# Performance work log

Hardware: AMD Instinct MI355X
Metric: run time of the kernel (lower is better)

## Reference

```python
import jax, jax.numpy as jnp
import numpy as np

NUM_GROUPS = 8   # num_groups1, recursive_index=False path
NUM_HEADS = 8


def setup_inputs() -> dict:
    key = jax.random.key(0)
    k1, k2, k3 = jax.random.split(key, 3)
    B, C, H, W = 4, 256, 64, 64
    x = jax.random.normal(k1, (B, C, H, W), dtype=jnp.float32)
    w_qkv = jax.random.normal(k2, (3 * C, C), dtype=jnp.float32) * 0.02
    w_proj = jax.random.normal(k3, (C, C), dtype=jnp.float32) * 0.02
    b_proj = jnp.zeros((C,), dtype=jnp.float32)
    return {"x": x, "w_qkv": w_qkv, "w_proj": w_proj, "b_proj": b_proj}


def reference(x, w_qkv, w_proj, b_proj):
    B, C, H, W = x.shape
    N = H * W
    G = NUM_GROUPS
    nh = NUM_HEADS
    hd = C // nh
    M = N // G
    scale = hd ** -0.5

    # b c h w -> b (h w) c
    xf = x.reshape(B, C, N).transpose(0, 2, 1)  # [B, N, C]

    # qkv linear (no bias), then split into groups / heads
    qkv = (xf @ w_qkv.T).reshape(B, G, M, 3, nh, hd)
    qkv = jnp.transpose(qkv, (3, 0, 1, 4, 2, 5))  # [3, B, G, nh, M, hd]
    q, k, v = qkv[0], qkv[1], qkv[2]

    # grouped multi-head attention, manual softmax
    attn = jax.nn.softmax(jnp.einsum('bghmd,bghnd->bghmn', q, k) * scale, axis=-1)
    out = jnp.einsum('bghmn,bghnd->bghmd', attn, v)

    # [B,G,nh,M,hd] -> [B,G,M,C] -> [B,N,C]
    out = out.transpose(0, 1, 3, 2, 4).reshape(B, N, C)

    out = out @ w_proj.T + b_proj

    # b (h w) c -> b c h w
    return out.transpose(0, 2, 1).reshape(B, C, H, W)
```

## Files before the change

### kernel.cpp

```cpp
#include <hip/hip_runtime.h>
#include <hip/hip_bf16.h>

#define Bb 4
#define Cc 256
#define Nn 4096
#define Gg 8
#define NHh 8
#define HDd 32
#define Mm 512

typedef __bf16 bf16_t;
typedef __bf16 bf16x2 __attribute__((ext_vector_type(2)));
typedef __bf16 bf16x4 __attribute__((ext_vector_type(4)));
typedef __bf16 bf16x8 __attribute__((ext_vector_type(8)));
typedef float f32x4 __attribute__((ext_vector_type(4)));

#define LSCALE (0.17677669529663687f * 1.44269504088896340f)

__device__ __forceinline__ void load_lds16(const bf16_t* g, bf16_t* l) {
  __builtin_amdgcn_global_load_lds(
      (const __attribute__((address_space(1))) void*)g,
      (__attribute__((address_space(3))) void*)l, 16, 0, 0);
}

__global__ __launch_bounds__(256) void prep_kernel(
    const float* __restrict__ x, bf16_t* __restrict__ xT,
    const float* __restrict__ wqkv, const float* __restrict__ wproj,
    bf16_t* __restrict__ wq_b, bf16_t* __restrict__ wp_b) {
  int bid = blockIdx.x, tid = threadIdx.x;
  if (bid >= 1024) {
    int i = (bid - 1024) * 256 + tid;
    wq_b[i] = (bf16_t)wqkv[i];
    if (i < Cc * Cc) wp_b[i] = (bf16_t)wproj[i];
    return;
  }
  __shared__ float t[64][65];
  int b = bid >> 8, c0 = ((bid >> 6) & 3) * 64, n0 = (bid & 63) * 64;
  const float* xp = x + ((long long)b * Cc + c0) * Nn + n0;
#pragma unroll
  for (int it = 0; it < 4; ++it) {
    int idx = it * 256 + tid;
    int r = idx >> 4, col = (idx & 15) * 4;
    f32x4 v = *(const f32x4*)&xp[(long long)r * Nn + col];
    t[r][col] = v[0];
    t[r][col + 1] = v[1];
    t[r][col + 2] = v[2];
    t[r][col + 3] = v[3];
  }
  __syncthreads();
  bf16_t* op = xT + ((long long)b * Nn + n0) * Cc + c0;
#pragma unroll
  for (int it = 0; it < 2; ++it) {
    int idx = it * 256 + tid;
    int n = idx >> 3, cg = (idx & 7) * 8;
    bf16x8 w;
#pragma unroll
    for (int j = 0; j < 8; ++j) w[j] = (bf16_t)t[cg + j][n];
    *(bf16x8*)&op[(long long)n * Cc + cg] = w;
  }
}

__global__ __launch_bounds__(256) void qkv_gemm_kernel(
    const bf16_t* __restrict__ xT, const bf16_t* __restrict__ wqb,
    bf16_t* __restrict__ Qh, bf16_t* __restrict__ Kh, bf16_t* __restrict__ Vh) {
  __shared__ bf16_t As[128 * 32];
  __shared__ bf16_t Bs[128 * 32];
  int bid = blockIdx.x;
  int tid = threadIdx.x, lane = tid & 63, wid = tid >> 6;
  int quad = lane >> 4, l16 = lane & 15;
  bool isQK = bid < 512;
  const bf16_t *A, *Bt;
  int m0, n0, z = 0;
  if (isQK) {
    m0 = (bid >> 2) * 128;
    n0 = (bid & 3) * 128;
    A = xT;
    Bt = wqb;
  } else {
    int vb = bid - 512;
    z = vb >> 6;
    int rem = vb & 63;
    m0 = (rem >> 5) * 128;
    n0 = (rem & 31) * 128;
    A = wqb + 512 * Cc;
    Bt = xT + (long long)z * Nn * Cc;
  }
  int wm = (wid >> 1) * 64, wn = (wid & 1) * 64;

  f32x4 acc[4][4];
#pragma unroll
  for (int i = 0; i < 4; ++i)
#pragma unroll
    for (int j = 0; j < 4; ++j) acc[i][j] = (f32x4){0.f, 0.f, 0.f, 0.f};

  int scol = (lane & 3) * 8;
  for (int k0 = 0; k0 < Cc; k0 += 32) {
    __syncthreads();
#pragma unroll
    for (int r = 0; r < 2; ++r) {
      int chunk = wid * 2 + r;
      int row = chunk * 16 + (lane >> 2);
      load_lds16(&A[(long long)(m0 + row) * Cc + k0 + scol], &As[chunk * 512]);
      load_lds16(&Bt[(long long)(n0 + row) * Cc + k0 + scol], &Bs[chunk * 512]);
    }
    __syncthreads();
    bf16x8 a[4], b[4];
#pragma unroll
    for (int i = 0; i < 4; ++i)
      a[i] = *(const bf16x8*)&As[(wm + i * 16 + l16) * 32 + quad * 8];
#pragma unroll
    for (int j = 0; j < 4; ++j)
      b[j] = *(const bf16x8*)&Bs[(wn + j * 16 + l16) * 32 + quad * 8];
#pragma unroll
    for (int i = 0; i < 4; ++i)
#pragma unroll
      for (int j = 0; j < 4; ++j)
        acc[i][j] = __builtin_amdgcn_mfma_f32_16x16x32_bf16(a[i], b[j], acc[i][j], 0, 0, 0);
  }

#pragma unroll
  for (int i = 0; i < 4; ++i) {
#pragma unroll
    for (int j = 0; j < 4; ++j) {
      int col = n0 + wn + j * 16 + l16;
#pragma unroll
      for (int r = 0; r < 4; ++r) {
        int row = m0 + wm + i * 16 + quad * 4 + r;
        float v = acc[i][j][r];
        if (isQK) {
          int bb = row >> 12, gg = (row >> 9) & 7, m = row & 511;
          int hh = (col >> 5) & 7, d = col & 31;
          long long hb = (long long)((bb << 6) | (gg << 3) | hh) * (Mm * HDd);
          if (col < 256)
            Qh[hb + m * HDd + d] = (bf16_t)(v * LSCALE);
          else
            Kh[hb + m * HDd + d] = (bf16_t)v;
        } else {
          int hh = row >> 5, d = row & 31, gg = col >> 9, m = col & 511;
          long long hb = (long long)((z << 6) | (gg << 3) | hh) * (Mm * HDd);
          Vh[hb + d * Mm + m] = (bf16_t)v;
        }
      }
    }
  }
}

__global__ __launch_bounds__(256, 2) void attn_kernel(
    const bf16_t* __restrict__ Qh, const bf16_t* __restrict__ Kh,
    const bf16_t* __restrict__ Vh, bf16_t* __restrict__ Oa) {
  __shared__ bf16_t Ks[512 * 32];
  __shared__ bf16_t Vs[32 * 520];
  int gid = blockIdx.x;
  int ms = gid & 1, head = gid >> 1;
  int h = head & 7, g = (head >> 3) & 7, b = head >> 6;
  int tid = threadIdx.x, lane = tid & 63, wid = tid >> 6;
  int quad = lane >> 4, l16 = lane & 15;

  const bf16_t* Kg = Kh + (long long)head * (Mm * HDd);
  const bf16_t* Vg = Vh + (long long)head * (Mm * HDd);
  const bf16_t* Qg = Qh + (long long)head * (Mm * HDd) + ms * 256 * HDd;

#pragma unroll
  for (int it = 0; it < 8; ++it) {
    int chunk = wid * 8 + it;
    load_lds16(&Kg[chunk * 512 + lane * 8], &Ks[chunk * 512]);
  }
#pragma unroll
  for (int it = 0; it < 8; ++it) {
    int d = wid * 8 + it;
    load_lds16(&Vg[d * Mm + lane * 8], &Vs[d * 520]);
  }
  __syncthreads();

  int rp0 = ((l16 >> 2) << 3) | (l16 & 3);
  const bf16_t* Kp0 = &Ks[rp0 * HDd + quad * 8];
  const bf16_t* Kp1 = Kp0 + 4 * HDd;
  const bf16_t* VsL = &Vs[l16 * 520 + quad * 8];
  const bf16_t* VsH = &Vs[(16 + l16) * 520 + quad * 8];
  const f32x4 zero = (f32x4){0.f, 0.f, 0.f, 0.f};

#pragma unroll 1
  for (int t = 0; t < 2; ++t) {
    int m0 = wid * 64 + t * 32;
    bf16x8 qa = *(const bf16x8*)&Qg[(m0 + l16) * HDd + quad * 8];
    bf16x8 qb = *(const bf16x8*)&Qg[(m0 + 16 + l16) * HDd + quad * 8];

    float sma = 0.f, smb = 0.f;
    f32x4 oLa = zero, oHa = zero, oLb = zero, oHb = zero;

#pragma unroll 4
    for (int c = 0; c < 16; ++c) {
      int nb = c * 32;
      bf16x8 kf0 = *(const bf16x8*)&Kp0[nb * HDd];
      bf16x8 kf1 = *(const bf16x8*)&Kp1[nb * HDd];
      f32x4 sa0 = __builtin_amdgcn_mfma_f32_16x16x32_bf16(kf0, qa, zero, 0, 0, 0);
      f32x4 sa1 = __builtin_amdgcn_mfma_f32_16x16x32_bf16(kf1, qa, zero, 0, 0, 0);
      f32x4 sb0 = __builtin_amdgcn_mfma_f32_16x16x32_bf16(kf0, qb, zero, 0, 0, 0);
      f32x4 sb1 = __builtin_amdgcn_mfma_f32_16x16x32_bf16(kf1, qb, zero, 0, 0, 0);
      bf16x8 pa, pb;
#pragma unroll
      for (int r = 0; r < 4; ++r) {
        float e0 = __builtin_exp2f(sa0[r]);
        float e1 = __builtin_exp2f(sa1[r]);
        sma += e0 + e1;
        pa[r] = (bf16_t)e0;
        pa[4 + r] = (bf16_t)e1;
        float f0 = __builtin_exp2f(sb0[r]);
        float f1 = __builtin_exp2f(sb1[r]);
        smb += f0 + f1;
        pb[r] = (bf16_t)f0;
        pb[4 + r] = (bf16_t)f1;
      }
      bf16x8 vL = *(const bf16x8*)&VsL[nb];
      bf16x8 vH = *(const bf16x8*)&VsH[nb];
      oLa = __builtin_amdgcn_mfma_f32_16x16x32_bf16(vL, pa, oLa, 0, 0, 0);
      oHa = __builtin_amdgcn_mfma_f32_16x16x32_bf16(vH, pa, oHa, 0, 0, 0);
      oLb = __builtin_amdgcn_mfma_f32_16x16x32_bf16(vL, pb, oLb, 0, 0, 0);
      oHb = __builtin_amdgcn_mfma_f32_16x16x32_bf16(vH, pb, oHb, 0, 0, 0);
    }

    sma += __shfl_xor(sma, 16, 64);
    sma += __shfl_xor(sma, 32, 64);
    smb += __shfl_xor(smb, 16, 64);
    smb += __shfl_xor(smb, 32, 64);
    float inva = 1.f / sma, invb = 1.f / smb;

    long long orowa =
        ((long long)(b * Nn + g * Mm + ms * 256 + m0 + l16)) * Cc + h * HDd;
    long long orowb = orowa + 16 * Cc;
    bf16x4 wLa, wHa, wLb, wHb;
#pragma unroll
    for (int r = 0; r < 4; ++r) {
      wLa[r] = (bf16_t)(oLa[r] * inva);
      wHa[r] = (bf16_t)(oHa[r] * inva);
      wLb[r] = (bf16_t)(oLb[r] * invb);
      wHb[r] = (bf16_t)(oHb[r] * invb);
    }
    *(bf16x4*)&Oa[orowa + quad * 4] = wLa;
    *(bf16x4*)&Oa[orowa + 16 + quad * 4] = wHa;
    *(bf16x4*)&Oa[orowb + quad * 4] = wLb;
    *(bf16x4*)&Oa[orowb + 16 + quad * 4] = wHb;
  }
}

__global__ __launch_bounds__(256) void proj_kernel(
    const bf16_t* __restrict__ Wp, const bf16_t* __restrict__ Oa,
    float* __restrict__ out, const float* __restrict__ bias) {
  __shared__ bf16_t As[128 * 32];
  __shared__ bf16_t Bs[128 * 32];
  int tid = threadIdx.x, lane = tid & 63, wid = tid >> 6;
  int quad = lane >> 4, l16 = lane & 15;
  int z = blockIdx.z;
  const bf16_t* Bt = Oa + (long long)z * Nn * Cc;
  int m0 = blockIdx.y * 128, n0 = blockIdx.x * 128;
  int wm = (wid >> 1) * 64, wn = (wid & 1) * 64;

  f32x4 acc[4][4];
#pragma unroll
  for (int i = 0; i < 4; ++i)
#pragma unroll
    for (int j = 0; j < 4; ++j) acc[i][j] = (f32x4){0.f, 0.f, 0.f, 0.f};

  int scol = (lane & 3) * 8;
  for (int k0 = 0; k0 < Cc; k0 += 32) {
    __syncthreads();
#pragma unroll
    for (int r = 0; r < 2; ++r) {
      int chunk = wid * 2 + r;
      int row = chunk * 16 + (lane >> 2);
      load_lds16(&Wp[(long long)(m0 + row) * Cc + k0 + scol], &As[chunk * 512]);
      load_lds16(&Bt[(long long)(n0 + row) * Cc + k0 + scol], &Bs[chunk * 512]);
    }
    __syncthreads();
    bf16x8 a[4], b[4];
#pragma unroll
    for (int i = 0; i < 4; ++i)
      a[i] = *(const bf16x8*)&As[(wm + i * 16 + l16) * 32 + quad * 8];
#pragma unroll
    for (int j = 0; j < 4; ++j)
      b[j] = *(const bf16x8*)&Bs[(wn + j * 16 + l16) * 32 + quad * 8];
#pragma unroll
    for (int i = 0; i < 4; ++i)
#pragma unroll
      for (int j = 0; j < 4; ++j)
        acc[i][j] = __builtin_amdgcn_mfma_f32_16x16x32_bf16(a[i], b[j], acc[i][j], 0, 0, 0);
  }

#pragma unroll
  for (int i = 0; i < 4; ++i) {
#pragma unroll
    for (int j = 0; j < 4; ++j) {
      int col = n0 + wn + j * 16 + l16;
#pragma unroll
      for (int r = 0; r < 4; ++r) {
        int row = m0 + wm + i * 16 + quad * 4 + r;
        out[(long long)z * (Cc * Nn) + (long long)row * Nn + col] =
            acc[i][j][r] + bias[row];
      }
    }
  }
}

extern "C" void kernel_launch(void* const* d_in, const int* in_sizes, int n_in,
                              void* d_out, int out_size, void* d_ws, size_t ws_size,
                              hipStream_t stream) {
  (void)in_sizes; (void)n_in; (void)out_size; (void)ws_size;
  const float* x = (const float*)d_in[0];
  const float* w_qkv = (const float*)d_in[1];
  const float* w_proj = (const float*)d_in[2];
  const float* b_proj = (const float*)d_in[3];
  float* out = (float*)d_out;

  char* ws = (char*)d_ws;
  bf16_t* xT  = (bf16_t*)(ws);
  bf16_t* wqb = (bf16_t*)(ws + 8388608);
  bf16_t* wpb = (bf16_t*)(ws + 8781824);
  bf16_t* Qh  = (bf16_t*)(ws + 8912896);
  bf16_t* Kh  = (bf16_t*)(ws + 17301504);
  bf16_t* Vh  = (bf16_t*)(ws + 25690112);
  bf16_t* Oa  = (bf16_t*)(ws + 34078720);

  prep_kernel<<<1792, 256, 0, stream>>>(x, xT, w_qkv, w_proj, wqb, wpb);
  qkv_gemm_kernel<<<768, 256, 0, stream>>>(xT, wqb, Qh, Kh, Vh);
  attn_kernel<<<512, 256, 0, stream>>>(Qh, Kh, Vh, Oa);
  proj_kernel<<<dim3(32, 2, 4), 256, 0, stream>>>(wpb, Oa, out, b_proj);
}
```

Baseline: 126.6 us.

## Double-buffer LDS tiles in GEMM kernels and preload Q fragments in attention

```diff
diff --git a/kernel.cpp b/kernel.cpp
--- a/kernel.cpp
+++ b/kernel.cpp
@@ -63,8 +63,8 @@
 __global__ __launch_bounds__(256) void qkv_gemm_kernel(
     const bf16_t* __restrict__ xT, const bf16_t* __restrict__ wqb,
     bf16_t* __restrict__ Qh, bf16_t* __restrict__ Kh, bf16_t* __restrict__ Vh) {
-  __shared__ bf16_t As[128 * 32];
-  __shared__ bf16_t Bs[128 * 32];
+  __shared__ bf16_t As[2][128 * 32];
+  __shared__ bf16_t Bs[2][128 * 32];
   int bid = blockIdx.x;
   int tid = threadIdx.x, lane = tid & 63, wid = tid >> 6;
   int quad = lane >> 4, l16 = lane & 15;
@@ -94,28 +94,35 @@
     for (int j = 0; j < 4; ++j) acc[i][j] = (f32x4){0.f, 0.f, 0.f, 0.f};
 
   int scol = (lane & 3) * 8;
-  for (int k0 = 0; k0 < Cc; k0 += 32) {
-    __syncthreads();
+  auto stage = [&](int bufi, int k0) {
 #pragma unroll
     for (int r = 0; r < 2; ++r) {
       int chunk = wid * 2 + r;
       int row = chunk * 16 + (lane >> 2);
-      load_lds16(&A[(long long)(m0 + row) * Cc + k0 + scol], &As[chunk * 512]);
-      load_lds16(&Bt[(long long)(n0 + row) * Cc + k0 + scol], &Bs[chunk * 512]);
-    }
-    __syncthreads();
+      load_lds16(&A[(long long)(m0 + row) * Cc + k0 + scol], &As[bufi][chunk * 512]);
+      load_lds16(&Bt[(long long)(n0 + row) * Cc + k0 + scol], &Bs[bufi][chunk * 512]);
+    }
+  };
+
+  stage(0, 0);
+  __syncthreads();
+  for (int t = 0; t < 8; ++t) {
+    if (t < 7) stage((t + 1) & 1, (t + 1) * 32);
+    const bf16_t* Ap = As[t & 1];
+    const bf16_t* Bp = Bs[t & 1];
     bf16x8 a[4], b[4];
 #pragma unroll
     for (int i = 0; i < 4; ++i)
-      a[i] = *(const bf16x8*)&As[(wm + i * 16 + l16) * 32 + quad * 8];
+      a[i] = *(const bf16x8*)&Ap[(wm + i * 16 + l16) * 32 + quad * 8];
 #pragma unroll
     for (int j = 0; j < 4; ++j)
-      b[j] = *(const bf16x8*)&Bs[(wn + j * 16 + l16) * 32 + quad * 8];
+      b[j] = *(const bf16x8*)&Bp[(wn + j * 16 + l16) * 32 + quad * 8];
 #pragma unroll
     for (int i = 0; i < 4; ++i)
 #pragma unroll
       for (int j = 0; j < 4; ++j)
         acc[i][j] = __builtin_amdgcn_mfma_f32_16x16x32_bf16(a[i], b[j], acc[i][j], 0, 0, 0);
+    __syncthreads();
   }
 
 #pragma unroll
@@ -170,6 +177,10 @@
     int d = wid * 8 + it;
     load_lds16(&Vg[d * Mm + lane * 8], &Vs[d * 520]);
   }
+  bf16x8 q0 = *(const bf16x8*)&Qg[(wid * 64 + 0 + l16) * HDd + quad * 8];
+  bf16x8 q1 = *(const bf16x8*)&Qg[(wid * 64 + 16 + l16) * HDd + quad * 8];
+  bf16x8 q2 = *(const bf16x8*)&Qg[(wid * 64 + 32 + l16) * HDd + quad * 8];
+  bf16x8 q3 = *(const bf16x8*)&Qg[(wid * 64 + 48 + l16) * HDd + quad * 8];
   __syncthreads();
 
   int rp0 = ((l16 >> 2) << 3) | (l16 & 3);
@@ -179,11 +190,11 @@
   const bf16_t* VsH = &Vs[(16 + l16) * 520 + quad * 8];
   const f32x4 zero = (f32x4){0.f, 0.f, 0.f, 0.f};
 
-#pragma unroll 1
+#pragma unroll
   for (int t = 0; t < 2; ++t) {
     int m0 = wid * 64 + t * 32;
-    bf16x8 qa = *(const bf16x8*)&Qg[(m0 + l16) * HDd + quad * 8];
-    bf16x8 qb = *(const bf16x8*)&Qg[(m0 + 16 + l16) * HDd + quad * 8];
+    bf16x8 qa = t ? q2 : q0;
+    bf16x8 qb = t ? q3 : q1;
 
     float sma = 0.f, smb = 0.f;
     f32x4 oLa = zero, oHa = zero, oLb = zero, oHb = zero;
@@ -246,8 +257,8 @@
 __global__ __launch_bounds__(256) void proj_kernel(
     const bf16_t* __restrict__ Wp, const bf16_t* __restrict__ Oa,
     float* __restrict__ out, const float* __restrict__ bias) {
-  __shared__ bf16_t As[128 * 32];
-  __shared__ bf16_t Bs[128 * 32];
+  __shared__ bf16_t As[2][128 * 32];
+  __shared__ bf16_t Bs[2][128 * 32];
   int tid = threadIdx.x, lane = tid & 63, wid = tid >> 6;
   int quad = lane >> 4, l16 = lane & 15;
   int z = blockIdx.z;
@@ -262,28 +273,35 @@
     for (int j = 0; j < 4; ++j) acc[i][j] = (f32x4){0.f, 0.f, 0.f, 0.f};
 
   int scol = (lane & 3) * 8;
-  for (int k0 = 0; k0 < Cc; k0 += 32) {
-    __syncthreads();
+  auto stage = [&](int bufi, int k0) {
 #pragma unroll
     for (int r = 0; r < 2; ++r) {
       int chunk = wid * 2 + r;
       int row = chunk * 16 + (lane >> 2);
-      load_lds16(&Wp[(long long)(m0 + row) * Cc + k0 + scol], &As[chunk * 512]);
-      load_lds16(&Bt[(long long)(n0 + row) * Cc + k0 + scol], &Bs[chunk * 512]);
-    }
-    __syncthreads();
+      load_lds16(&Wp[(long long)(m0 + row) * Cc + k0 + scol], &As[bufi][chunk * 512]);
+      load_lds16(&Bt[(long long)(n0 + row) * Cc + k0 + scol], &Bs[bufi][chunk * 512]);
+    }
+  };
+
+  stage(0, 0);
+  __syncthreads();
+  for (int t = 0; t < 8; ++t) {
+    if (t < 7) stage((t + 1) & 1, (t + 1) * 32);
+    const bf16_t* Ap = As[t & 1];
+    const bf16_t* Bp = Bs[t & 1];
     bf16x8 a[4], b[4];
 #pragma unroll
     for (int i = 0; i < 4; ++i)
-      a[i] = *(const bf16x8*)&As[(wm + i * 16 + l16) * 32 + quad * 8];
+      a[i] = *(const bf16x8*)&Ap[(wm + i * 16 + l16) * 32 + quad * 8];
 #pragma unroll
     for (int j = 0; j < 4; ++j)
-      b[j] = *(const bf16x8*)&Bs[(wn + j * 16 + l16) * 32 + quad * 8];
+      b[j] = *(const bf16x8*)&Bp[(wn + j * 16 + l16) * 32 + quad * 8];
 #pragma unroll
     for (int i = 0; i < 4; ++i)
 #pragma unroll
       for (int j = 0; j < 4; ++j)
         acc[i][j] = __builtin_amdgcn_mfma_f32_16x16x32_bf16(a[i], b[j], acc[i][j], 0, 0, 0);
+    __syncthreads();
   }
 
 #pragma unroll
```

After: 125.0 us. About the same (-1.3%).
